# Kernel tuning notes

Hardware: AMD Instinct MI355X
Metric: run time of the kernel (lower is better)

The kernel has to match this reference:

```python
import jax, jax.numpy as jnp
import numpy as np

N_NODES = 50000
N_EDGES = 800000
IN_CH = 128
OUT_CH = 64
HEADS = 1
NEG_SLOPE = 0.2

def _glorot(key, shape):
    stdv = np.sqrt(6.0 / (shape[-2] + shape[-1]))
    return jax.random.uniform(key, shape, jnp.float32, -stdv, stdv)

def setup_inputs() -> dict:
    key = jax.random.key(0)
    k1, k2, k3, k4, k5 = jax.random.split(key, 5)
    x = jax.random.normal(k1, (N_NODES, IN_CH), jnp.float32)
    src = jax.random.randint(k2, (N_EDGES,), 0, N_NODES)
    dst = jax.random.randint(k3, (N_EDGES,), 0, N_NODES)
    # ensure no pre-existing self loops (remove_self_loops is then identity)
    dst = jnp.where(src == dst, (dst + 1) % N_NODES, dst)
    edge_index = jnp.stack([src, dst]).astype(jnp.int64)
    weight = _glorot(k4, (IN_CH, HEADS * OUT_CH))
    att = _glorot(k5, (1, HEADS, 2 * OUT_CH))
    bias = jnp.zeros((OUT_CH,), jnp.float32)
    return {"x": x, "edge_index": edge_index, "weight": weight, "att": att, "bias": bias}

def reference(x, edge_index, weight, att, bias):
    N = x.shape[0]
    # linear projection -> [N, heads, out]
    h = (x @ weight).reshape(N, HEADS, OUT_CH)
    # add self loops (input guaranteed free of self loops)
    loops = jnp.arange(N, dtype=edge_index.dtype)
    src = jnp.concatenate([edge_index[0], loops])  # source j
    dst = jnp.concatenate([edge_index[1], loops])  # target i
    x_j = h[src]   # [E+N, heads, out]
    x_i = h[dst]
    # attention logits: (cat([x_i, x_j]) * att).sum(-1) -> [E+N, heads]
    alpha = jnp.concatenate([x_i, x_j], axis=-1)
    alpha = (alpha * att).sum(axis=-1)
    alpha = jax.nn.leaky_relu(alpha, NEG_SLOPE)
    # segment softmax over destination nodes
    amax = jax.ops.segment_max(alpha, dst, num_segments=N)
    e = jnp.exp(alpha - amax[dst])
    esum = jax.ops.segment_sum(e, dst, num_segments=N)
    alpha = e / (esum[dst] + 1e-16)
    # message + scatter-add aggregation
    msg = x_j * alpha[:, :, None]
    out = jax.ops.segment_sum(msg, dst, num_segments=N)  # [N, heads, out]
    out = out.mean(axis=1) + bias
    # F.normalize (L2, dim=1, eps=1e-12); dropout is eval-mode identity
    norm = jnp.maximum(jnp.linalg.norm(out, axis=1, keepdims=True), 1e-12)
    return out / norm
```

## Files before the change

### kernel.cpp

```cpp
#include <hip/hip_runtime.h>
#include <math.h>

#define IN_CH 128
#define OUT_CH 64
#define NEG_SLOPE 0.2f
#define CAP 64
#define NSHARD 8
#define CHUNK_EDGES 4096

typedef long long ll2 __attribute__((ext_vector_type(2)));

__device__ __forceinline__ unsigned short f2bf(float f) {
    unsigned u = __float_as_uint(f);
    unsigned r = (u + 0x7FFFu + ((u >> 16) & 1u)) >> 16;
    return (unsigned short)r;
}

__device__ __forceinline__ bool sniff_is64(const void* edges) {
    const unsigned* up = (const unsigned*)edges;
    bool is64 = true;
#pragma unroll
    for (int k = 0; k < 16; k++) is64 = is64 && (up[2 * k + 1] == 0u);
    return is64;
}

__global__ __launch_bounds__(256) void k_mm_cs(
        const float* __restrict__ x, const float* __restrict__ W,
        const float* __restrict__ att, unsigned short* __restrict__ h16,
        float* __restrict__ asrc, float* __restrict__ adst, int N,
        const void* __restrict__ edges, int* __restrict__ counts,
        int* __restrict__ slots, int* __restrict__ oflow_cnt,
        int2* __restrict__ oflow, int E, int mmb, int nchunks,
        int* __restrict__ queues) {
    __shared__ float Ws[IN_CH * OUT_CH];
    int t = threadIdx.x;
    int bid = blockIdx.x;
    int total = gridDim.x;
    int mbefore = (int)(((long long)bid * mmb) / total);
    int mafter  = (int)(((long long)(bid + 1) * mmb) / total);
    bool ismm = (mafter != mbefore);
    int id = mbefore;

    if (!ismm) {
        int* chunk_sh = (int*)Ws;
        int xcd;
        asm volatile("s_getreg_b32 %0, hwreg(HW_REG_XCC_ID)" : "=s"(xcd));
        xcd &= 7;
        int lo = (int)(((long long)xcd * N) / NSHARD);
        int hi = (int)(((long long)(xcd + 1) * N) / NSHARD);
        bool is64 = sniff_is64(edges);
        for (;;) {
            if (t == 0)
                *chunk_sh = __hip_atomic_fetch_add(queues + xcd * 16, 1,
                                                   __ATOMIC_RELAXED,
                                                   __HIP_MEMORY_SCOPE_WORKGROUP);
            __syncthreads();
            int chunk = *chunk_sh;
            __syncthreads();
            if (chunk >= nchunks) return;

            int base = chunk * CHUNK_EDGES + t * 16;
            int nv = E - base;
            if (nv <= 0) continue;
            if (nv > 16) nv = 16;
            int dv[16], sv[16];
            if (nv == 16) {
                if (is64) {
                    const ll2* pd = (const ll2*)((const long long*)edges +
                                                 (size_t)E + base);
                    const ll2* ps = (const ll2*)((const long long*)edges + base);
#pragma unroll
                    for (int i = 0; i < 8; i++) {
                        ll2 w = pd[i];
                        dv[2 * i] = (int)w.x; dv[2 * i + 1] = (int)w.y;
                    }
#pragma unroll
                    for (int i = 0; i < 8; i++) {
                        ll2 v = ps[i];
                        sv[2 * i] = (int)v.x; sv[2 * i + 1] = (int)v.y;
                    }
                } else {
                    const int4* pd = (const int4*)((const int*)edges + E + base);
                    const int4* ps = (const int4*)((const int*)edges + base);
#pragma unroll
                    for (int i = 0; i < 4; i++) {
                        int4 w = pd[i];
                        dv[4 * i] = w.x; dv[4 * i + 1] = w.y;
                        dv[4 * i + 2] = w.z; dv[4 * i + 3] = w.w;
                    }
#pragma unroll
                    for (int i = 0; i < 4; i++) {
                        int4 v = ps[i];
                        sv[4 * i] = v.x; sv[4 * i + 1] = v.y;
                        sv[4 * i + 2] = v.z; sv[4 * i + 3] = v.w;
                    }
                }
            } else {
                for (int i = 0; i < 16; i++) {
                    if (i < nv) {
                        if (is64) {
                            dv[i] = (int)((const long long*)edges)[(size_t)E + base + i];
                            sv[i] = (int)((const long long*)edges)[base + i];
                        } else {
                            dv[i] = ((const int*)edges)[E + base + i];
                            sv[i] = ((const int*)edges)[base + i];
                        }
                    } else {
                        dv[i] = -1; sv[i] = 0;
                    }
                }
            }
#pragma unroll
            for (int i = 0; i < 16; i++) {
                int d = dv[i];
                if (d >= lo && d < hi) {
                    int r = __hip_atomic_fetch_add(counts + d, 1, __ATOMIC_RELAXED,
                                                   __HIP_MEMORY_SCOPE_WORKGROUP);
                    if (r < CAP) {
                        slots[((size_t)d << 6) + r] = sv[i];
                    } else {
                        int p2 = atomicAdd(oflow_cnt, 1);
                        oflow[p2] = make_int2(sv[i], d);
                    }
                }
            }
        }
    }

    for (int i = t * 4; i < IN_CH * OUT_CH; i += 256 * 4)
        *(float4*)&Ws[i] = *(const float4*)&W[i];
    int cg = t & 15, g = t >> 4;
    float4 att_d = *(const float4*)&att[cg * 4];
    float4 att_s = *(const float4*)&att[64 + cg * 4];
    __syncthreads();

    int n0 = id * 64 + g * 4;
    int nn[4];
#pragma unroll
    for (int m = 0; m < 4; m++) nn[m] = min(n0 + m, N - 1);

    float4 acc[4];
#pragma unroll
    for (int m = 0; m < 4; m++) acc[m] = make_float4(0.f, 0.f, 0.f, 0.f);

#pragma unroll 2
    for (int k4 = 0; k4 < IN_CH / 4; k4++) {
        float4 xv[4];
#pragma unroll
        for (int m = 0; m < 4; m++)
            xv[m] = *(const float4*)&x[(size_t)nn[m] * IN_CH + k4 * 4];
        float4 wv[4];
#pragma unroll
        for (int j = 0; j < 4; j++)
            wv[j] = *(const float4*)&Ws[(k4 * 4 + j) * OUT_CH + cg * 4];
#pragma unroll
        for (int m = 0; m < 4; m++) {
            acc[m].x = fmaf(xv[m].x, wv[0].x, acc[m].x);
            acc[m].y = fmaf(xv[m].x, wv[0].y, acc[m].y);
            acc[m].z = fmaf(xv[m].x, wv[0].z, acc[m].z);
            acc[m].w = fmaf(xv[m].x, wv[0].w, acc[m].w);
            acc[m].x = fmaf(xv[m].y, wv[1].x, acc[m].x);
            acc[m].y = fmaf(xv[m].y, wv[1].y, acc[m].y);
            acc[m].z = fmaf(xv[m].y, wv[1].z, acc[m].z);
            acc[m].w = fmaf(xv[m].y, wv[1].w, acc[m].w);
            acc[m].x = fmaf(xv[m].z, wv[2].x, acc[m].x);
            acc[m].y = fmaf(xv[m].z, wv[2].y, acc[m].y);
            acc[m].z = fmaf(xv[m].z, wv[2].z, acc[m].z);
            acc[m].w = fmaf(xv[m].z, wv[2].w, acc[m].w);
            acc[m].x = fmaf(xv[m].w, wv[3].x, acc[m].x);
            acc[m].y = fmaf(xv[m].w, wv[3].y, acc[m].y);
            acc[m].z = fmaf(xv[m].w, wv[3].z, acc[m].z);
            acc[m].w = fmaf(xv[m].w, wv[3].w, acc[m].w);
        }
    }

#pragma unroll
    for (int m = 0; m < 4; m++) {
        int node = n0 + m;
        if (node < N) {
            ushort4 hv;
            hv.x = f2bf(acc[m].x);
            hv.y = f2bf(acc[m].y);
            hv.z = f2bf(acc[m].z);
            hv.w = f2bf(acc[m].w);
            *(ushort4*)&h16[(size_t)node * OUT_CH + cg * 4] = hv;
        }
        float pd = acc[m].x * att_d.x + acc[m].y * att_d.y +
                   acc[m].z * att_d.z + acc[m].w * att_d.w;
        float ps = acc[m].x * att_s.x + acc[m].y * att_s.y +
                   acc[m].z * att_s.z + acc[m].w * att_s.w;
#pragma unroll
        for (int msk = 1; msk < 16; msk <<= 1) {
            pd += __shfl_xor(pd, msk, 64);
            ps += __shfl_xor(ps, msk, 64);
        }
        if (cg == 0 && node < N) { adst[node] = pd; asrc[node] = ps; }
    }
}

__global__ __launch_bounds__(256) void k_agg(const unsigned short* __restrict__ h16,
                                             const int* __restrict__ slots,
                                             const int* __restrict__ counts,
                                             const int* __restrict__ oflow_cnt,
                                             const int2* __restrict__ oflow,
                                             const float* __restrict__ asrc,
                                             const float* __restrict__ adst,
                                             const float* __restrict__ bias,
                                             float* __restrict__ out, int N) {
    __shared__ float2 stage[4][64];
    int lane = threadIdx.x & 63;
    int wid = threadIdx.x >> 6;
    int node = blockIdx.x * 4 + wid;
    if (node >= N) return;
    int half = lane >> 5;
    int ch2 = (lane & 31) * 2;

    float aD = adst[node];
    float a = aD + asrc[node];
    a = a > 0.f ? a : NEG_SLOPE * a;
    float w_self = __expf(a);
    unsigned hv = *(const unsigned*)&h16[(size_t)node * OUT_CH + ch2];
    float wse = half ? 0.f : w_self;
    float accx = wse * __uint_as_float(hv << 16);
    float accy = wse * __uint_as_float(hv & 0xFFFF0000u);

    int c = counts[node];
    int cs = min(c, CAP);
    int sv = 0;
    float wv = 0.f;
    if (lane < cs) {
        sv = slots[((size_t)node << 6) + lane];
        float av = aD + asrc[sv];
        av = av > 0.f ? av : NEG_SLOPE * av;
        wv = __expf(av);
    }
    float esum_lane = wv;
    stage[wid][lane] = make_float2(__int_as_float(sv), wv);

    for (int j = 0; j < cs; j += 16) {
#pragma unroll
        for (int k = 0; k < 8; k++) {
            float2 p = stage[wid][j + 2 * k + half];
            int s = __float_as_int(p.x);
            unsigned v = *(const unsigned*)&h16[((size_t)s << 6) + ch2];
            accx = fmaf(p.y, __uint_as_float(v << 16), accx);
            accy = fmaf(p.y, __uint_as_float(v & 0xFFFF0000u), accy);
        }
    }
    accx += __shfl_xor(accx, 32, 64);
    accy += __shfl_xor(accy, 32, 64);
#pragma unroll
    for (int m = 32; m >= 1; m >>= 1) esum_lane += __shfl_xor(esum_lane, m, 64);
    float esum = esum_lane + w_self;

    int oc = *oflow_cnt;
    if (oc > 0) {
        for (int i = 0; i < oc; i++) {
            int2 e = oflow[i];
            if (e.y == node) {
                float av = aD + asrc[e.x];
                av = av > 0.f ? av : NEG_SLOPE * av;
                float w = __expf(av);
                esum += w;
                unsigned v = *(const unsigned*)&h16[((size_t)e.x << 6) + ch2];
                accx = fmaf(w, __uint_as_float(v << 16), accx);
                accy = fmaf(w, __uint_as_float(v & 0xFFFF0000u), accy);
            }
        }
    }

    float inv = 1.f / (esum + 1e-16f);
    float2 bv = *(const float2*)&bias[ch2];
    float vx = accx * inv + bv.x;
    float vy = accy * inv + bv.y;
    float ss = vx * vx + vy * vy;
#pragma unroll
    for (int m = 16; m >= 1; m >>= 1) ss += __shfl_xor(ss, m, 64);
    float rinv = 1.f / fmaxf(sqrtf(ss), 1e-12f);
    if (!half)
        *(float2*)&out[(size_t)node * OUT_CH + ch2] = make_float2(vx * rinv, vy * rinv);
}

extern "C" void kernel_launch(void* const* d_in, const int* in_sizes, int n_in,
                              void* d_out, int out_size, void* d_ws, size_t ws_size,
                              hipStream_t stream) {
    const float* x    = (const float*)d_in[0];
    const void*  edges = d_in[1];
    const float* W    = (const float*)d_in[2];
    const float* att  = (const float*)d_in[3];
    const float* bias = (const float*)d_in[4];
    float* out = (float*)d_out;

    const int N = in_sizes[0] / IN_CH;
    const int E = in_sizes[1] / 2;
    const int NCHUNKS = (E + CHUNK_EDGES - 1) / CHUNK_EDGES;
    const int MMB = (N + 63) / 64;
    const int CSB = NSHARD * NCHUNKS;
    const int grid = MMB + CSB;

    char* ws = (char*)d_ws;
    size_t off = 0;
    auto alloc = [&](size_t bytes) -> void* {
        void* p = ws + off;
        off += bytes;
        off = (off + 255) & ~(size_t)255;
        return p;
    };
    int*            counts   = (int*)alloc((size_t)(N + 256) * 4);
    int*            slots    = (int*)alloc((size_t)N * CAP * 4);
    int2*           oflow    = (int2*)alloc((size_t)E * 8);
    unsigned short* h16      = (unsigned short*)alloc((size_t)N * OUT_CH * 2);
    float*          asrc     = (float*)alloc((size_t)N * 4);
    float*          adst     = (float*)alloc((size_t)N * 4);
    int*            oflow_cnt = counts + N;
    int*            queues    = counts + N + 64;

    hipMemsetAsync(counts, 0, (size_t)(N + 256) * 4, stream);
    k_mm_cs<<<grid, 256, 0, stream>>>(x, W, att, h16, asrc, adst, N,
                                      edges, counts, slots, oflow_cnt,
                                      oflow, E, MMB, NCHUNKS, queues);
    k_agg<<<(N + 3) / 4, 256, 0, stream>>>(h16, slots, counts, oflow_cnt, oflow,
                                           asrc, adst, bias, out, N);
}
```

Baseline: 160.5 us.

## Pre-bucket edges by destination shard before XCD-local slot filling

```diff
diff --git a/kernel.cpp b/kernel.cpp
--- a/kernel.cpp
+++ b/kernel.cpp
@@ -9,6 +9,9 @@
 #define CHUNK_EDGES 4096
 
 typedef long long ll2 __attribute__((ext_vector_type(2)));
+typedef int i4v __attribute__((ext_vector_type(4)));
+typedef float f4v __attribute__((ext_vector_type(4)));
+typedef unsigned short us4v __attribute__((ext_vector_type(4)));
 
 __device__ __forceinline__ unsigned short f2bf(float f) {
     unsigned u = __float_as_uint(f);
@@ -24,103 +27,163 @@
     return is64;
 }
 
+__global__ __launch_bounds__(256) void k_bucket(
+        const void* __restrict__ edges, int E, int S,
+        int2* __restrict__ bucket, int bcap, int* __restrict__ bucket_cnt) {
+    __shared__ unsigned short hist[256][NSHARD];
+    __shared__ int base_sh[NSHARD];
+    int t = threadIdx.x;
+    int base = blockIdx.x * CHUNK_EDGES + t * 16;
+    bool is64 = sniff_is64(edges);
+    int sv[16], dv[16];
+    int nv = E - base;
+    if (nv > 16) nv = 16;
+    if (nv < 0) nv = 0;
+    if (nv == 16) {
+        if (is64) {
+            const ll2* ps = (const ll2*)((const long long*)edges + base);
+            const ll2* pd = (const ll2*)((const long long*)edges + (size_t)E + base);
+#pragma unroll
+            for (int i = 0; i < 8; i++) {
+                ll2 v = __builtin_nontemporal_load(ps + i);
+                sv[2 * i] = (int)v.x; sv[2 * i + 1] = (int)v.y;
+            }
+#pragma unroll
+            for (int i = 0; i < 8; i++) {
+                ll2 w = __builtin_nontemporal_load(pd + i);
+                dv[2 * i] = (int)w.x; dv[2 * i + 1] = (int)w.y;
+            }
+        } else {
+            const i4v* ps = (const i4v*)((const int*)edges + base);
+            const i4v* pd = (const i4v*)((const int*)edges + E + base);
+#pragma unroll
+            for (int i = 0; i < 4; i++) {
+                i4v v = __builtin_nontemporal_load(ps + i);
+                sv[4 * i] = v.x; sv[4 * i + 1] = v.y;
+                sv[4 * i + 2] = v.z; sv[4 * i + 3] = v.w;
+            }
+#pragma unroll
+            for (int i = 0; i < 4; i++) {
+                i4v w = __builtin_nontemporal_load(pd + i);
+                dv[4 * i] = w.x; dv[4 * i + 1] = w.y;
+                dv[4 * i + 2] = w.z; dv[4 * i + 3] = w.w;
+            }
+        }
+    } else {
+        for (int i = 0; i < 16; i++) {
+            if (i < nv) {
+                if (is64) {
+                    sv[i] = (int)((const long long*)edges)[base + i];
+                    dv[i] = (int)((const long long*)edges)[(size_t)E + base + i];
+                } else {
+                    sv[i] = ((const int*)edges)[base + i];
+                    dv[i] = ((const int*)edges)[E + base + i];
+                }
+            } else { sv[i] = 0; dv[i] = 0; }
+        }
+    }
+    int bv[16];
+    int tcnt[NSHARD];
+#pragma unroll
+    for (int b = 0; b < NSHARD; b++) tcnt[b] = 0;
+#pragma unroll
+    for (int i = 0; i < 16; i++) {
+        int b = (i < nv) ? (int)((unsigned)dv[i] / (unsigned)S) : -1;
+        bv[i] = b;
+#pragma unroll
+        for (int bb = 0; bb < NSHARD; bb++) tcnt[bb] += (b == bb);
+    }
+#pragma unroll
+    for (int b = 0; b < NSHARD; b++) hist[t][b] = (unsigned short)tcnt[b];
+    __syncthreads();
+    if (t < NSHARD) {
+        int run = 0;
+        for (int i = 0; i < 256; i++) {
+            int c = hist[i][t];
+            hist[i][t] = (unsigned short)run;
+            run += c;
+        }
+        base_sh[t] = atomicAdd(bucket_cnt + t * 16, run);
+    }
+    __syncthreads();
+    int off[NSHARD];
+#pragma unroll
+    for (int b = 0; b < NSHARD; b++) off[b] = base_sh[b] + (int)hist[t][b];
+#pragma unroll
+    for (int i = 0; i < 16; i++) {
+        if (i < nv) {
+            int b = bv[i];
+#pragma unroll
+            for (int bb = 0; bb < NSHARD; bb++) {
+                if (b == bb) {
+                    bucket[(size_t)bb * bcap + off[bb]] = make_int2(sv[i], dv[i]);
+                    off[bb]++;
+                }
+            }
+        }
+    }
+}
+
 __global__ __launch_bounds__(256) void k_mm_cs(
         const float* __restrict__ x, const float* __restrict__ W,
         const float* __restrict__ att, unsigned short* __restrict__ h16,
         float* __restrict__ asrc, float* __restrict__ adst, int N,
-        const void* __restrict__ edges, int* __restrict__ counts,
+        const int2* __restrict__ bucket, int bcap,
+        const int* __restrict__ bucket_cnt, int* __restrict__ counts,
         int* __restrict__ slots, int* __restrict__ oflow_cnt,
-        int2* __restrict__ oflow, int E, int mmb, int nchunks,
-        int* __restrict__ queues) {
+        int2* __restrict__ oflow, int mmb,
+        int* __restrict__ queues, int* __restrict__ mmq) {
     __shared__ float Ws[IN_CH * OUT_CH];
+    __shared__ int grab_sh;
     int t = threadIdx.x;
-    int bid = blockIdx.x;
-    int total = gridDim.x;
-    int mbefore = (int)(((long long)bid * mmb) / total);
-    int mafter  = (int)(((long long)(bid + 1) * mmb) / total);
-    bool ismm = (mafter != mbefore);
-    int id = mbefore;
-
-    if (!ismm) {
-        int* chunk_sh = (int*)Ws;
-        int xcd;
-        asm volatile("s_getreg_b32 %0, hwreg(HW_REG_XCC_ID)" : "=s"(xcd));
-        xcd &= 7;
-        int lo = (int)(((long long)xcd * N) / NSHARD);
-        int hi = (int)(((long long)(xcd + 1) * N) / NSHARD);
-        bool is64 = sniff_is64(edges);
-        for (;;) {
-            if (t == 0)
-                *chunk_sh = __hip_atomic_fetch_add(queues + xcd * 16, 1,
+
+    int xcd;
+    asm volatile("s_getreg_b32 %0, hwreg(HW_REG_XCC_ID)" : "=s"(xcd));
+    xcd &= 7;
+    int cnt = bucket_cnt[xcd * 16];
+    int nchunks = (cnt + CHUNK_EDGES - 1) / CHUNK_EDGES;
+    const int2* mybkt = bucket + (size_t)xcd * bcap;
+    for (;;) {
+        if (t == 0)
+            grab_sh = __hip_atomic_fetch_add(queues + xcd * 16, 1,
+                                             __ATOMIC_RELAXED,
+                                             __HIP_MEMORY_SCOPE_WORKGROUP);
+        __syncthreads();
+        int chunk = grab_sh;
+        __syncthreads();
+        if (chunk >= nchunks) break;
+        int base = chunk * CHUNK_EDGES + t * 16;
+        int nv = cnt - base;
+        if (nv > 16) nv = 16;
+        if (nv > 0) {
+            int2 ev[16];
+            if (nv == 16) {
+                const i4v* p = (const i4v*)(mybkt + base);
+#pragma unroll
+                for (int i = 0; i < 8; i++) {
+                    i4v q = p[i];
+                    ev[2 * i] = make_int2(q.x, q.y);
+                    ev[2 * i + 1] = make_int2(q.z, q.w);
+                }
+            } else {
+                for (int i = 0; i < 16; i++)
+                    if (i < nv) ev[i] = mybkt[base + i];
+            }
+            int rr[16];
+#pragma unroll
+            for (int i = 0; i < 16; i++)
+                if (i < nv)
+                    rr[i] = __hip_atomic_fetch_add(counts + ev[i].y, 1,
                                                    __ATOMIC_RELAXED,
                                                    __HIP_MEMORY_SCOPE_WORKGROUP);
-            __syncthreads();
-            int chunk = *chunk_sh;
-            __syncthreads();
-            if (chunk >= nchunks) return;
-
-            int base = chunk * CHUNK_EDGES + t * 16;
-            int nv = E - base;
-            if (nv <= 0) continue;
-            if (nv > 16) nv = 16;
-            int dv[16], sv[16];
-            if (nv == 16) {
-                if (is64) {
-                    const ll2* pd = (const ll2*)((const long long*)edges +
-                                                 (size_t)E + base);
-                    const ll2* ps = (const ll2*)((const long long*)edges + base);
-#pragma unroll
-                    for (int i = 0; i < 8; i++) {
-                        ll2 w = pd[i];
-                        dv[2 * i] = (int)w.x; dv[2 * i + 1] = (int)w.y;
-                    }
-#pragma unroll
-                    for (int i = 0; i < 8; i++) {
-                        ll2 v = ps[i];
-                        sv[2 * i] = (int)v.x; sv[2 * i + 1] = (int)v.y;
-                    }
-                } else {
-                    const int4* pd = (const int4*)((const int*)edges + E + base);
-                    const int4* ps = (const int4*)((const int*)edges + base);
-#pragma unroll
-                    for (int i = 0; i < 4; i++) {
-                        int4 w = pd[i];
-                        dv[4 * i] = w.x; dv[4 * i + 1] = w.y;
-                        dv[4 * i + 2] = w.z; dv[4 * i + 3] = w.w;
-                    }
-#pragma unroll
-                    for (int i = 0; i < 4; i++) {
-                        int4 v = ps[i];
-                        sv[4 * i] = v.x; sv[4 * i + 1] = v.y;
-                        sv[4 * i + 2] = v.z; sv[4 * i + 3] = v.w;
-                    }
-                }
-            } else {
-                for (int i = 0; i < 16; i++) {
-                    if (i < nv) {
-                        if (is64) {
-                            dv[i] = (int)((const long long*)edges)[(size_t)E + base + i];
-                            sv[i] = (int)((const long long*)edges)[base + i];
-                        } else {
-                            dv[i] = ((const int*)edges)[E + base + i];
-                            sv[i] = ((const int*)edges)[base + i];
-                        }
-                    } else {
-                        dv[i] = -1; sv[i] = 0;
-                    }
-                }
-            }
 #pragma unroll
             for (int i = 0; i < 16; i++) {
-                int d = dv[i];
-                if (d >= lo && d < hi) {
-                    int r = __hip_atomic_fetch_add(counts + d, 1, __ATOMIC_RELAXED,
-                                                   __HIP_MEMORY_SCOPE_WORKGROUP);
-                    if (r < CAP) {
-                        slots[((size_t)d << 6) + r] = sv[i];
+                if (i < nv) {
+                    if (rr[i] < CAP) {
+                        slots[((size_t)ev[i].y << 6) + rr[i]] = ev[i].x;
                     } else {
                         int p2 = atomicAdd(oflow_cnt, 1);
-                        oflow[p2] = make_int2(sv[i], d);
+                        oflow[p2] = make_int2(ev[i].x, ev[i].y);
                     }
                 }
             }
@@ -134,67 +197,77 @@
     float4 att_s = *(const float4*)&att[64 + cg * 4];
     __syncthreads();
 
-    int n0 = id * 64 + g * 4;
-    int nn[4];
-#pragma unroll
-    for (int m = 0; m < 4; m++) nn[m] = min(n0 + m, N - 1);
-
-    float4 acc[4];
-#pragma unroll
-    for (int m = 0; m < 4; m++) acc[m] = make_float4(0.f, 0.f, 0.f, 0.f);
+    for (;;) {
+        if (t == 0) grab_sh = atomicAdd(mmq, 1);
+        __syncthreads();
+        int id = grab_sh;
+        __syncthreads();
+        if (id >= mmb) return;
+
+        int n0 = id * 64 + g * 4;
+        int nn[4];
+#pragma unroll
+        for (int m = 0; m < 4; m++) nn[m] = min(n0 + m, N - 1);
+
+        float4 acc[4];
+#pragma unroll
+        for (int m = 0; m < 4; m++) acc[m] = make_float4(0.f, 0.f, 0.f, 0.f);
 
 #pragma unroll 2
-    for (int k4 = 0; k4 < IN_CH / 4; k4++) {
-        float4 xv[4];
-#pragma unroll
-        for (int m = 0; m < 4; m++)
-            xv[m] = *(const float4*)&x[(size_t)nn[m] * IN_CH + k4 * 4];
-        float4 wv[4];
-#pragma unroll
-        for (int j = 0; j < 4; j++)
-            wv[j] = *(const float4*)&Ws[(k4 * 4 + j) * OUT_CH + cg * 4];
+        for (int k4 = 0; k4 < IN_CH / 4; k4++) {
+            f4v xv[4];
+#pragma unroll
+            for (int m = 0; m < 4; m++)
+                xv[m] = __builtin_nontemporal_load(
+                    (const f4v*)&x[(size_t)nn[m] * IN_CH + k4 * 4]);
+            float4 wv[4];
+#pragma unroll
+            for (int j = 0; j < 4; j++)
+                wv[j] = *(const float4*)&Ws[(k4 * 4 + j) * OUT_CH + cg * 4];
+#pragma unroll
+            for (int m = 0; m < 4; m++) {
+                acc[m].x = fmaf(xv[m].x, wv[0].x, acc[m].x);
+                acc[m].y = fmaf(xv[m].x, wv[0].y, acc[m].y);
+                acc[m].z = fmaf(xv[m].x, wv[0].z, acc[m].z);
+                acc[m].w = fmaf(xv[m].x, wv[0].w, acc[m].w);
+                acc[m].x = fmaf(xv[m].y, wv[1].x, acc[m].x);
+                acc[m].y = fmaf(xv[m].y, wv[1].y, acc[m].y);
+                acc[m].z = fmaf(xv[m].y, wv[1].z, acc[m].z);
+                acc[m].w = fmaf(xv[m].y, wv[1].w, acc[m].w);
+                acc[m].x = fmaf(xv[m].z, wv[2].x, acc[m].x);
+                acc[m].y = fmaf(xv[m].z, wv[2].y, acc[m].y);
+                acc[m].z = fmaf(xv[m].z, wv[2].z, acc[m].z);
+                acc[m].w = fmaf(xv[m].z, wv[2].w, acc[m].w);
+                acc[m].x = fmaf(xv[m].w, wv[3].x, acc[m].x);
+                acc[m].y = fmaf(xv[m].w, wv[3].y, acc[m].y);
+                acc[m].z = fmaf(xv[m].w, wv[3].z, acc[m].z);
+                acc[m].w = fmaf(xv[m].w, wv[3].w, acc[m].w);
+            }
+        }
+
 #pragma unroll
         for (int m = 0; m < 4; m++) {
-            acc[m].x = fmaf(xv[m].x, wv[0].x, acc[m].x);
-            acc[m].y = fmaf(xv[m].x, wv[0].y, acc[m].y);
-            acc[m].z = fmaf(xv[m].x, wv[0].z, acc[m].z);
-            acc[m].w = fmaf(xv[m].x, wv[0].w, acc[m].w);
-            acc[m].x = fmaf(xv[m].y, wv[1].x, acc[m].x);
-            acc[m].y = fmaf(xv[m].y, wv[1].y, acc[m].y);
-            acc[m].z = fmaf(xv[m].y, wv[1].z, acc[m].z);
-            acc[m].w = fmaf(xv[m].y, wv[1].w, acc[m].w);
-            acc[m].x = fmaf(xv[m].z, wv[2].x, acc[m].x);
-            acc[m].y = fmaf(xv[m].z, wv[2].y, acc[m].y);
-            acc[m].z = fmaf(xv[m].z, wv[2].z, acc[m].z);
-            acc[m].w = fmaf(xv[m].z, wv[2].w, acc[m].w);
-            acc[m].x = fmaf(xv[m].w, wv[3].x, acc[m].x);
-            acc[m].y = fmaf(xv[m].w, wv[3].y, acc[m].y);
-            acc[m].z = fmaf(xv[m].w, wv[3].z, acc[m].z);
-            acc[m].w = fmaf(xv[m].w, wv[3].w, acc[m].w);
-        }
-    }
-
-#pragma unroll
-    for (int m = 0; m < 4; m++) {
-        int node = n0 + m;
-        if (node < N) {
-            ushort4 hv;
-            hv.x = f2bf(acc[m].x);
-            hv.y = f2bf(acc[m].y);
-            hv.z = f2bf(acc[m].z);
-            hv.w = f2bf(acc[m].w);
-            *(ushort4*)&h16[(size_t)node * OUT_CH + cg * 4] = hv;
-        }
-        float pd = acc[m].x * att_d.x + acc[m].y * att_d.y +
-                   acc[m].z * att_d.z + acc[m].w * att_d.w;
-        float ps = acc[m].x * att_s.x + acc[m].y * att_s.y +
-                   acc[m].z * att_s.z + acc[m].w * att_s.w;
-#pragma unroll
-        for (int msk = 1; msk < 16; msk <<= 1) {
-            pd += __shfl_xor(pd, msk, 64);
-            ps += __shfl_xor(ps, msk, 64);
-        }
-        if (cg == 0 && node < N) { adst[node] = pd; asrc[node] = ps; }
+            int node = n0 + m;
+            if (node < N) {
+                us4v hv;
+                hv.x = f2bf(acc[m].x);
+                hv.y = f2bf(acc[m].y);
+                hv.z = f2bf(acc[m].z);
+                hv.w = f2bf(acc[m].w);
+                __builtin_nontemporal_store(
+                    hv, (us4v*)&h16[(size_t)node * OUT_CH + cg * 4]);
+            }
+            float pd = acc[m].x * att_d.x + acc[m].y * att_d.y +
+                       acc[m].z * att_d.z + acc[m].w * att_d.w;
+            float ps = acc[m].x * att_s.x + acc[m].y * att_s.y +
+                       acc[m].z * att_s.z + acc[m].w * att_s.w;
+#pragma unroll
+            for (int msk = 1; msk < 16; msk <<= 1) {
+                pd += __shfl_xor(pd, msk, 64);
+                ps += __shfl_xor(ps, msk, 64);
+            }
+            if (cg == 0 && node < N) { adst[node] = pd; asrc[node] = ps; }
+        }
     }
 }
 
@@ -293,10 +366,11 @@
 
     const int N = in_sizes[0] / IN_CH;
     const int E = in_sizes[1] / 2;
-    const int NCHUNKS = (E + CHUNK_EDGES - 1) / CHUNK_EDGES;
+    const int S = (N + NSHARD - 1) / NSHARD;
     const int MMB = (N + 63) / 64;
-    const int CSB = NSHARD * NCHUNKS;
-    const int grid = MMB + CSB;
+    const int BKB = (E + CHUNK_EDGES - 1) / CHUNK_EDGES;
+    const int bcap = E / NSHARD + 16384;
+    const int grid1 = MMB + 256;
 
     char* ws = (char*)d_ws;
     size_t off = 0;
@@ -306,19 +380,23 @@
         off = (off + 255) & ~(size_t)255;
         return p;
     };
-    int*            counts   = (int*)alloc((size_t)(N + 256) * 4);
+    int*            counts   = (int*)alloc((size_t)(N + 384) * 4);
     int*            slots    = (int*)alloc((size_t)N * CAP * 4);
-    int2*           oflow    = (int2*)alloc((size_t)E * 8);
+    int2*           oflow    = (int2*)alloc((size_t)65536 * 8);
     unsigned short* h16      = (unsigned short*)alloc((size_t)N * OUT_CH * 2);
     float*          asrc     = (float*)alloc((size_t)N * 4);
     float*          adst     = (float*)alloc((size_t)N * 4);
-    int*            oflow_cnt = counts + N;
-    int*            queues    = counts + N + 64;
-
-    hipMemsetAsync(counts, 0, (size_t)(N + 256) * 4, stream);
-    k_mm_cs<<<grid, 256, 0, stream>>>(x, W, att, h16, asrc, adst, N,
-                                      edges, counts, slots, oflow_cnt,
-                                      oflow, E, MMB, NCHUNKS, queues);
+    int2*           bucket   = (int2*)alloc((size_t)NSHARD * bcap * 8);
+    int*            oflow_cnt  = counts + N;
+    int*            queues     = counts + N + 64;
+    int*            bucket_cnt = counts + N + 192;
+    int*            mmq        = counts + N + 320;
+
+    hipMemsetAsync(counts, 0, (size_t)(N + 384) * 4, stream);
+    k_bucket<<<BKB, 256, 0, stream>>>(edges, E, S, bucket, bcap, bucket_cnt);
+    k_mm_cs<<<grid1, 256, 0, stream>>>(x, W, att, h16, asrc, adst, N,
+                                       bucket, bcap, bucket_cnt, counts,
+                                       slots, oflow_cnt, oflow, MMB, queues, mmq);
     k_agg<<<(N + 3) / 4, 256, 0, stream>>>(h16, slots, counts, oflow_cnt, oflow,
                                            asrc, adst, bias, out, N);
 }
```

New measurement: 183.8 us. 1.15x slower.

## Replace sharded global-atomic CSR build with two-pass bucket sort using LDS counters

Applied to the files above, without the earlier changes.

```diff
diff --git a/kernel.cpp b/kernel.cpp
--- a/kernel.cpp
+++ b/kernel.cpp
@@ -5,10 +5,12 @@
 #define OUT_CH 64
 #define NEG_SLOPE 0.2f
 #define CAP 64
-#define NSHARD 8
+#define BSHIFT 8
+#define BS 256
 #define CHUNK_EDGES 4096
 
 typedef long long ll2 __attribute__((ext_vector_type(2)));
+typedef int i4v __attribute__((ext_vector_type(4)));
 
 __device__ __forceinline__ unsigned short f2bf(float f) {
     unsigned u = __float_as_uint(f);
@@ -24,107 +26,117 @@
     return is64;
 }
 
+__global__ __launch_bounds__(256) void k_bucket(
+        const void* __restrict__ edges, int E, int nbkt,
+        int2* __restrict__ bucket, int bcap, int* __restrict__ bucket_cnt) {
+    __shared__ int lcur[256];
+    __shared__ int lbase[256];
+    int t = threadIdx.x;
+    lcur[t] = 0;
+    __syncthreads();
+
+    int base = blockIdx.x * CHUNK_EDGES + t * 16;
+    bool is64 = sniff_is64(edges);
+    int sv[16], dv[16], rr[16];
+    int nv = E - base;
+    if (nv > 16) nv = 16;
+    if (nv < 0) nv = 0;
+    if (nv == 16) {
+        if (is64) {
+            const ll2* ps = (const ll2*)((const long long*)edges + base);
+            const ll2* pd = (const ll2*)((const long long*)edges + (size_t)E + base);
+#pragma unroll
+            for (int i = 0; i < 8; i++) {
+                ll2 v = __builtin_nontemporal_load(ps + i);
+                sv[2 * i] = (int)v.x; sv[2 * i + 1] = (int)v.y;
+            }
+#pragma unroll
+            for (int i = 0; i < 8; i++) {
+                ll2 w = __builtin_nontemporal_load(pd + i);
+                dv[2 * i] = (int)w.x; dv[2 * i + 1] = (int)w.y;
+            }
+        } else {
+            const i4v* ps = (const i4v*)((const int*)edges + base);
+            const i4v* pd = (const i4v*)((const int*)edges + E + base);
+#pragma unroll
+            for (int i = 0; i < 4; i++) {
+                i4v v = __builtin_nontemporal_load(ps + i);
+                sv[4 * i] = v.x; sv[4 * i + 1] = v.y;
+                sv[4 * i + 2] = v.z; sv[4 * i + 3] = v.w;
+            }
+#pragma unroll
+            for (int i = 0; i < 4; i++) {
+                i4v w = __builtin_nontemporal_load(pd + i);
+                dv[4 * i] = w.x; dv[4 * i + 1] = w.y;
+                dv[4 * i + 2] = w.z; dv[4 * i + 3] = w.w;
+            }
+        }
+    } else {
+        for (int i = 0; i < 16; i++) {
+            if (i < nv) {
+                if (is64) {
+                    sv[i] = (int)((const long long*)edges)[base + i];
+                    dv[i] = (int)((const long long*)edges)[(size_t)E + base + i];
+                } else {
+                    sv[i] = ((const int*)edges)[base + i];
+                    dv[i] = ((const int*)edges)[E + base + i];
+                }
+            } else { sv[i] = 0; dv[i] = 0; }
+        }
+    }
+#pragma unroll
+    for (int i = 0; i < 16; i++)
+        if (i < nv) rr[i] = atomicAdd(&lcur[(unsigned)dv[i] >> BSHIFT], 1);
+    __syncthreads();
+    if (t < nbkt && lcur[t] > 0) lbase[t] = atomicAdd(bucket_cnt + t, lcur[t]);
+    __syncthreads();
+#pragma unroll
+    for (int i = 0; i < 16; i++) {
+        if (i < nv) {
+            int b = (unsigned)dv[i] >> BSHIFT;
+            bucket[(size_t)b * bcap + lbase[b] + rr[i]] = make_int2(sv[i], dv[i]);
+        }
+    }
+}
+
 __global__ __launch_bounds__(256) void k_mm_cs(
         const float* __restrict__ x, const float* __restrict__ W,
         const float* __restrict__ att, unsigned short* __restrict__ h16,
         float* __restrict__ asrc, float* __restrict__ adst, int N,
-        const void* __restrict__ edges, int* __restrict__ counts,
+        const int2* __restrict__ bucket, int bcap,
+        const int* __restrict__ bucket_cnt, int* __restrict__ counts,
         int* __restrict__ slots, int* __restrict__ oflow_cnt,
-        int2* __restrict__ oflow, int E, int mmb, int nchunks,
-        int* __restrict__ queues) {
+        int2* __restrict__ oflow, int mmb, int csb) {
     __shared__ float Ws[IN_CH * OUT_CH];
     int t = threadIdx.x;
     int bid = blockIdx.x;
-    int total = gridDim.x;
-    int mbefore = (int)(((long long)bid * mmb) / total);
-    int mafter  = (int)(((long long)(bid + 1) * mmb) / total);
-    bool ismm = (mafter != mbefore);
-    int id = mbefore;
-
-    if (!ismm) {
-        int* chunk_sh = (int*)Ws;
-        int xcd;
-        asm volatile("s_getreg_b32 %0, hwreg(HW_REG_XCC_ID)" : "=s"(xcd));
-        xcd &= 7;
-        int lo = (int)(((long long)xcd * N) / NSHARD);
-        int hi = (int)(((long long)(xcd + 1) * N) / NSHARD);
-        bool is64 = sniff_is64(edges);
-        for (;;) {
-            if (t == 0)
-                *chunk_sh = __hip_atomic_fetch_add(queues + xcd * 16, 1,
-                                                   __ATOMIC_RELAXED,
-                                                   __HIP_MEMORY_SCOPE_WORKGROUP);
-            __syncthreads();
-            int chunk = *chunk_sh;
-            __syncthreads();
-            if (chunk >= nchunks) return;
-
-            int base = chunk * CHUNK_EDGES + t * 16;
-            int nv = E - base;
-            if (nv <= 0) continue;
-            if (nv > 16) nv = 16;
-            int dv[16], sv[16];
-            if (nv == 16) {
-                if (is64) {
-                    const ll2* pd = (const ll2*)((const long long*)edges +
-                                                 (size_t)E + base);
-                    const ll2* ps = (const ll2*)((const long long*)edges + base);
-#pragma unroll
-                    for (int i = 0; i < 8; i++) {
-                        ll2 w = pd[i];
-                        dv[2 * i] = (int)w.x; dv[2 * i + 1] = (int)w.y;
-                    }
-#pragma unroll
-                    for (int i = 0; i < 8; i++) {
-                        ll2 v = ps[i];
-                        sv[2 * i] = (int)v.x; sv[2 * i + 1] = (int)v.y;
-                    }
-                } else {
-                    const int4* pd = (const int4*)((const int*)edges + E + base);
-                    const int4* ps = (const int4*)((const int*)edges + base);
-#pragma unroll
-                    for (int i = 0; i < 4; i++) {
-                        int4 w = pd[i];
-                        dv[4 * i] = w.x; dv[4 * i + 1] = w.y;
-                        dv[4 * i + 2] = w.z; dv[4 * i + 3] = w.w;
-                    }
-#pragma unroll
-                    for (int i = 0; i < 4; i++) {
-                        int4 v = ps[i];
-                        sv[4 * i] = v.x; sv[4 * i + 1] = v.y;
-                        sv[4 * i + 2] = v.z; sv[4 * i + 3] = v.w;
-                    }
-                }
+    int total = mmb + csb;
+    int cbefore = (int)(((long long)bid * csb) / total);
+    int cafter  = (int)(((long long)(bid + 1) * csb) / total);
+    bool iscs = (cafter != cbefore);
+    int id = iscs ? cbefore : (bid - cbefore);
+
+    if (iscs) {
+        int* lcnt = (int*)Ws;
+        int lo = id << BSHIFT;
+        lcnt[t] = 0;
+        __syncthreads();
+        int cnt = bucket_cnt[id];
+        const int2* mybkt = bucket + (size_t)id * bcap;
+        for (int idx = t; idx < cnt; idx += 256) {
+            int2 e = mybkt[idx];
+            int r = atomicAdd(&lcnt[e.y - lo], 1);
+            if (r < CAP) {
+                slots[((size_t)e.y << 6) + r] = e.x;
             } else {
-                for (int i = 0; i < 16; i++) {
-                    if (i < nv) {
-                        if (is64) {
-                            dv[i] = (int)((const long long*)edges)[(size_t)E + base + i];
-                            sv[i] = (int)((const long long*)edges)[base + i];
-                        } else {
-                            dv[i] = ((const int*)edges)[E + base + i];
-                            sv[i] = ((const int*)edges)[base + i];
-                        }
-                    } else {
-                        dv[i] = -1; sv[i] = 0;
-                    }
-                }
-            }
-#pragma unroll
-            for (int i = 0; i < 16; i++) {
-                int d = dv[i];
-                if (d >= lo && d < hi) {
-                    int r = __hip_atomic_fetch_add(counts + d, 1, __ATOMIC_RELAXED,
-                                                   __HIP_MEMORY_SCOPE_WORKGROUP);
-                    if (r < CAP) {
-                        slots[((size_t)d << 6) + r] = sv[i];
-                    } else {
-                        int p2 = atomicAdd(oflow_cnt, 1);
-                        oflow[p2] = make_int2(sv[i], d);
-                    }
-                }
-            }
-        }
+                int p2 = atomicAdd(oflow_cnt, 1);
+                oflow[p2] = e;
+            }
+        }
+        __syncthreads();
+        int node = lo + t;
+        if (node < N) counts[node] = lcnt[t];
+        return;
     }
 
     for (int i = t * 4; i < IN_CH * OUT_CH; i += 256 * 4)
@@ -293,10 +305,10 @@
 
     const int N = in_sizes[0] / IN_CH;
     const int E = in_sizes[1] / 2;
-    const int NCHUNKS = (E + CHUNK_EDGES - 1) / CHUNK_EDGES;
+    const int NBKT = (N + BS - 1) / BS;
     const int MMB = (N + 63) / 64;
-    const int CSB = NSHARD * NCHUNKS;
-    const int grid = MMB + CSB;
+    const int BKB = (E + CHUNK_EDGES - 1) / CHUNK_EDGES;
+    const int bcap = E / NBKT + 2048;
 
     char* ws = (char*)d_ws;
     size_t off = 0;
@@ -306,19 +318,22 @@
         off = (off + 255) & ~(size_t)255;
         return p;
     };
-    int*            counts   = (int*)alloc((size_t)(N + 256) * 4);
+    int*            ctrl     = (int*)alloc(320 * 4);
+    int*            counts   = (int*)alloc((size_t)N * 4);
     int*            slots    = (int*)alloc((size_t)N * CAP * 4);
-    int2*           oflow    = (int2*)alloc((size_t)E * 8);
+    int2*           oflow    = (int2*)alloc((size_t)65536 * 8);
     unsigned short* h16      = (unsigned short*)alloc((size_t)N * OUT_CH * 2);
     float*          asrc     = (float*)alloc((size_t)N * 4);
     float*          adst     = (float*)alloc((size_t)N * 4);
-    int*            oflow_cnt = counts + N;
-    int*            queues    = counts + N + 64;
-
-    hipMemsetAsync(counts, 0, (size_t)(N + 256) * 4, stream);
-    k_mm_cs<<<grid, 256, 0, stream>>>(x, W, att, h16, asrc, adst, N,
-                                      edges, counts, slots, oflow_cnt,
-                                      oflow, E, MMB, NCHUNKS, queues);
+    int2*           bucket   = (int2*)alloc((size_t)NBKT * bcap * 8);
+    int*            bucket_cnt = ctrl;
+    int*            oflow_cnt  = ctrl + 256;
+
+    hipMemsetAsync(ctrl, 0, 320 * 4, stream);
+    k_bucket<<<BKB, 256, 0, stream>>>(edges, E, NBKT, bucket, bcap, bucket_cnt);
+    k_mm_cs<<<MMB + NBKT, 256, 0, stream>>>(x, W, att, h16, asrc, adst, N,
+                                            bucket, bcap, bucket_cnt, counts,
+                                            slots, oflow_cnt, oflow, MMB, NBKT);
     k_agg<<<(N + 3) / 4, 256, 0, stream>>>(h16, slots, counts, oflow_cnt, oflow,
                                            asrc, adst, bias, out, N);
 }
```

Result: faster. 139.8 us (-12.9%).
